# Optimization experiments

Hardware: AMD Instinct MI355X
Metric: run time of the kernel (lower is better)

## Reference

```python
import jax, jax.numpy as jnp
import numpy as np

ALPHA = jnp.full((8,), 0.25, dtype=jnp.float32)  # per-class focal alpha
GAMMA = 2.0
TEMP = 0.07
CIRC_TARGET = 1.0
CIRC_WEIGHT = 0.1
MIN_AGREE = 0.6
W_FOCAL, W_CONTRAST, W_CONSENSUS = 1.0, 0.5, 0.3


def setup_inputs() -> dict:
    key = jax.random.key(0)
    k1, k2, k3, k4, k5 = jax.random.split(key, 5)
    return {
        "logits": jax.random.normal(k1, (32, 8, 256, 256), dtype=jnp.float32),
        "target": jax.random.randint(k2, (32, 256, 256), 0, 8, dtype=jnp.int32),
        "features": jax.random.normal(k3, (1024, 512), dtype=jnp.float32),
        "masks": jax.random.uniform(k4, (32, 3, 256, 256), dtype=jnp.float32),
        "method_preds": jax.random.uniform(k5, (3, 32, 256, 256), dtype=jnp.float32),
    }


def focal_loss(logits, target):
    B, C, H, W = logits.shape
    x = logits.transpose(0, 2, 3, 1).reshape(-1, C)  # [BHW, C]
    t = target.reshape(-1)
    logp = jax.nn.log_softmax(x, axis=-1)
    ce = -jnp.take_along_axis(logp, t[:, None], axis=1)[:, 0]
    p = jnp.exp(-ce)
    focal_w = ALPHA[t] * (1.0 - p) ** GAMMA
    return jnp.mean(focal_w * ce)


def contrastive_loss(features):
    Bf = features.shape[0]
    f = features / jnp.linalg.norm(features, axis=1, keepdims=True)
    sim = (f @ f.T) / TEMP  # [Bf, Bf]
    # default labels = arange(Bf//2) tiled twice -> each sample has exactly one
    # positive: its paired view at index (i + Bf//2) % Bf
    pos_idx = (jnp.arange(Bf) + Bf // 2) % Bf
    pos = sim[jnp.arange(Bf), pos_idx]
    diag = jnp.eye(Bf, dtype=bool)
    # logits row i = {positive_i} U negatives_i = all j != i (single positive case)
    masked = jnp.where(diag, -1e30, sim)
    lse = jax.nn.logsumexp(masked, axis=1)
    return jnp.mean(lse - pos)  # CE with target = the (only) positive


def circularity_loss(masks):
    m = masks[:, 0]  # [B, H, W] core channel
    B = m.shape[0]
    area = jnp.sum(m, axis=(1, 2))
    ex = jnp.sum(jnp.abs(m[:, 1:, :] - m[:, :-1, :]), axis=(1, 2))
    ey = jnp.sum(jnp.abs(m[:, :, 1:] - m[:, :, :-1]), axis=(1, 2))
    per = ex + ey
    circ = 4.0 * np.pi * area / jnp.maximum(per, 1e-12) ** 2
    li = jnp.where((area > 0) & (per > 0), (circ - CIRC_TARGET) ** 2, 0.0)
    return CIRC_WEIGHT * jnp.sum(li) / B


def consensus_loss(method_preds):
    K = method_preds.shape[0]
    total, n = 0.0, 0
    for i in range(K):  # K=3 methods -> 3 pairs (fixed, small)
        for j in range(i + 1, K):
            pi, pj = method_preds[i], method_preds[j]
            inter = jnp.sum(pi * pj)
            union = jnp.sum(pi + pj - pi * pj)
            iou = inter / (union + 1e-6)
            total = total + jax.nn.relu(MIN_AGREE - iou)
            n += 1
    return total / n


def reference(logits, target, features, masks, method_preds):
    return (W_FOCAL * focal_loss(logits, target)
            + W_CONTRAST * contrastive_loss(features)
            + circularity_loss(masks)
            + W_CONSENSUS * consensus_loss(method_preds))
```

## Files before the change

kernel.cpp:

```cpp
#include <hip/hip_runtime.h>
#include <math.h>

#define WS_FOCALP 0
#define WS_CONSP  2048
#define WS_AREAP  14336
#define WS_EXP_   14848
#define WS_EYP_   15360
#define WS_POS    15872
#define WS_PART   16896
#define WS_HI_B   393216
#define WS_LO_B   1441792

typedef __attribute__((ext_vector_type(8))) short bf16x8;
typedef __attribute__((ext_vector_type(4))) float f32x4;

#define MFMA16(a, b, c) __builtin_amdgcn_mfma_f32_16x16x32_bf16((a), (b), (c), 0, 0, 0)

__device__ inline float wave_reduce(float v) {
#pragma unroll
  for (int m = 32; m >= 1; m >>= 1) v += __shfl_xor(v, m);
  return v;
}

__device__ inline unsigned short bf16_rne(float x) {
  union { float f; unsigned u; } v; v.f = x;
  unsigned r = v.u + 0x7FFF + ((v.u >> 16) & 1);
  return (unsigned short)(r >> 16);
}
__device__ inline float bf16_f(unsigned short h) {
  union { unsigned u; float f; } v; v.u = ((unsigned)h) << 16; return v.f;
}

__device__ inline float focal_px(float v0, float v1, float v2, float v3,
                                 float v4, float v5, float v6, float v7, int tt) {
  float mx = fmaxf(fmaxf(fmaxf(v0, v1), fmaxf(v2, v3)),
                   fmaxf(fmaxf(v4, v5), fmaxf(v6, v7)));
  float se = __expf(v0 - mx) + __expf(v1 - mx) + __expf(v2 - mx) + __expf(v3 - mx) +
             __expf(v4 - mx) + __expf(v5 - mx) + __expf(v6 - mx) + __expf(v7 - mx);
  float xt = v0;
  xt = (tt == 1) ? v1 : xt;
  xt = (tt == 2) ? v2 : xt;
  xt = (tt == 3) ? v3 : xt;
  xt = (tt == 4) ? v4 : xt;
  xt = (tt == 5) ? v5 : xt;
  xt = (tt == 6) ? v6 : xt;
  xt = (tt == 7) ? v7 : xt;
  float lp = (xt - mx) - __logf(se);
  float p = __expf(lp);
  float om = 1.0f - p;
  return 0.25f * om * om * (-lp);
}

__global__ __launch_bounds__(256) void mega_kernel(
    const float* __restrict__ logits, const int* __restrict__ target,
    const float* __restrict__ feat, const float* __restrict__ masks,
    const float* __restrict__ preds, float* __restrict__ ws) {
  __shared__ float red[32];
  const int bid = blockIdx.x;
  const int tid = threadIdx.x;
  const int lane = tid & 63;
  const int wid = tid >> 6;

  if (bid < 2048) {
    int t = bid * 256 + tid;
    int p4 = t * 4;
    int b = p4 >> 16;
    int hw = p4 & 65535;
    const float* lb = logits + (b << 19) + hw;
    float4 x0 = *(const float4*)(lb + (0 << 16));
    float4 x1 = *(const float4*)(lb + (1 << 16));
    float4 x2 = *(const float4*)(lb + (2 << 16));
    float4 x3 = *(const float4*)(lb + (3 << 16));
    float4 x4 = *(const float4*)(lb + (4 << 16));
    float4 x5 = *(const float4*)(lb + (5 << 16));
    float4 x6 = *(const float4*)(lb + (6 << 16));
    float4 x7 = *(const float4*)(lb + (7 << 16));
    int4 tg = *(const int4*)(target + p4);
    float acc = 0.0f;
    acc += focal_px(x0.x, x1.x, x2.x, x3.x, x4.x, x5.x, x6.x, x7.x, tg.x);
    acc += focal_px(x0.y, x1.y, x2.y, x3.y, x4.y, x5.y, x6.y, x7.y, tg.y);
    acc += focal_px(x0.z, x1.z, x2.z, x3.z, x4.z, x5.z, x6.z, x7.z, tg.z);
    acc += focal_px(x0.w, x1.w, x2.w, x3.w, x4.w, x5.w, x6.w, x7.w, tg.w);
    float v = wave_reduce(acc);
    if (lane == 0) red[wid] = v;
    __syncthreads();
    if (tid == 0) ws[WS_FOCALP + bid] = red[0] + red[1] + red[2] + red[3];

  } else if (bid < 2560) {
    int bi = bid - 2048;
    int img = bi >> 4;
    int part = bi & 15;
    const float* mS = masks + img * 3 * 65536;
    const float4* m4 = (const float4*)mS;
    float a = 0.0f, ex = 0.0f, ey = 0.0f;
#pragma unroll
    for (int i = 0; i < 4; i++) {
      int v = tid + 256 * i;
      int rl = v >> 6;
      int c4 = v & 63;
      int row = part * 16 + rl;
      float4 val = m4[row * 64 + c4];
      a += val.x + val.y + val.z + val.w;
      ey += fabsf(val.y - val.x) + fabsf(val.z - val.y) + fabsf(val.w - val.z);
      if (c4 > 0) ey += fabsf(val.x - mS[row * 256 + c4 * 4 - 1]);
      if (row > 0) {
        float4 u = m4[(row - 1) * 64 + c4];
        ex += fabsf(val.x - u.x) + fabsf(val.y - u.y) +
              fabsf(val.z - u.z) + fabsf(val.w - u.w);
      }
    }
    float ra = wave_reduce(a);
    float rx = wave_reduce(ex);
    float ry = wave_reduce(ey);
    if (lane == 0) {
      red[wid + 0] = ra; red[wid + 4] = rx; red[wid + 8] = ry;
    }
    __syncthreads();
    if (tid == 0) {
      ws[WS_AREAP + bi] = red[0] + red[1] + red[2] + red[3];
      ws[WS_EXP_ + bi] = red[4] + red[5] + red[6] + red[7];
      ws[WS_EYP_ + bi] = red[8] + red[9] + red[10] + red[11];
    }

  } else if (bid < 4608) {
    int b = bid - 2560;
    int t = b * 256 + tid;
    const float4* q = (const float4*)preds;
    float4 a0 = q[t];
    float4 a1 = q[t + 524288];
    float4 a2 = q[t + 1048576];
    float s0 = a0.x + a0.y + a0.z + a0.w;
    float s1 = a1.x + a1.y + a1.z + a1.w;
    float s2 = a2.x + a2.y + a2.z + a2.w;
    float p01 = a0.x * a1.x + a0.y * a1.y + a0.z * a1.z + a0.w * a1.w;
    float p02 = a0.x * a2.x + a0.y * a2.y + a0.z * a2.z + a0.w * a2.w;
    float p12 = a1.x * a2.x + a1.y * a2.y + a1.z * a2.z + a1.w * a2.w;
    float r0 = wave_reduce(s0);
    float r1 = wave_reduce(s1);
    float r2 = wave_reduce(s2);
    float r3 = wave_reduce(p01);
    float r4 = wave_reduce(p02);
    float r5 = wave_reduce(p12);
    if (lane == 0) {
      red[wid + 0] = r0; red[wid + 4] = r1; red[wid + 8] = r2;
      red[wid + 12] = r3; red[wid + 16] = r4; red[wid + 20] = r5;
    }
    __syncthreads();
    if (tid == 0) {
#pragma unroll
      for (int k = 0; k < 6; k++)
        ws[WS_CONSP + k * 2048 + b] =
            red[k * 4] + red[k * 4 + 1] + red[k * 4 + 2] + red[k * 4 + 3];
    }

  } else {
    int row = (bid - 4608) * 4 + wid;
    const float4* f4 = (const float4*)feat;
    float4 u = f4[row * 128 + lane];
    float4 w = f4[row * 128 + 64 + lane];
    float s = u.x * u.x + u.y * u.y + u.z * u.z + u.w * u.w +
              w.x * w.x + w.y * w.y + w.z * w.z + w.w * w.w;
    s = wave_reduce(s);
    float scale = 3.7796447300922719f / sqrtf(s);
    float g[8] = {u.x * scale, u.y * scale, u.z * scale, u.w * scale,
                  w.x * scale, w.y * scale, w.z * scale, w.w * scale};
    unsigned short h[8];
    unsigned short l[8];
#pragma unroll
    for (int i = 0; i < 8; i++) {
      h[i] = bf16_rne(g[i]);
      l[i] = bf16_rne(g[i] - bf16_f(h[i]));
    }
    const int rg = row >> 4, r15 = row & 15;
    int k0 = lane * 4;
    int k1 = 256 + lane * 4;
    int off0 = (rg * 16 + (k0 >> 5)) * 1024 + (((k0 >> 3) & 3) * 16 + r15) * 16 + (k0 & 7) * 2;
    int off1 = (rg * 16 + (k1 >> 5)) * 1024 + (((k1 >> 3) & 3) * 16 + r15) * 16 + (k1 & 7) * 2;
    char* hb = (char*)ws + WS_HI_B;
    char* lb = (char*)ws + WS_LO_B;
    *(ushort4*)(hb + off0) = make_ushort4(h[0], h[1], h[2], h[3]);
    *(ushort4*)(hb + off1) = make_ushort4(h[4], h[5], h[6], h[7]);
    *(ushort4*)(lb + off0) = make_ushort4(l[0], l[1], l[2], l[3]);
    *(ushort4*)(lb + off1) = make_ushort4(l[4], l[5], l[6], l[7]);
  }
}

__global__ __launch_bounds__(256) void sim_kernel(float* __restrict__ ws) {
  const int tid = threadIdx.x;
  const int lane = tid & 63;
  const int wid = tid >> 6;
  const int rt = blockIdx.x >> 4, ct = blockIdx.x & 15;
  const int wr = wid >> 1, wc = wid & 1;
  const int l15 = lane & 15;
  const int hi8 = lane >> 4;
  const char* HI = (const char*)ws + WS_HI_B;
  const char* LO = (const char*)ws + WS_LO_B;
  const int rga = rt * 2 + wr;
  const int rgb = ct * 4 + wc * 2;
  const int lb16 = lane * 16;
  const char* pAh = HI + rga * 16384 + lb16;
  const char* pAl = LO + rga * 16384 + lb16;
  const char* pB0h = HI + rgb * 16384 + lb16;
  const char* pB0l = LO + rgb * 16384 + lb16;
  const char* pB1h = HI + (rgb + 1) * 16384 + lb16;
  const char* pB1l = LO + (rgb + 1) * 16384 + lb16;

  f32x4 acc0 = {0.f, 0.f, 0.f, 0.f};
  f32x4 acc1 = {0.f, 0.f, 0.f, 0.f};

  bf16x8 Aah0, Aal0, Abh00, Abl00, Abh10, Abl10;
  bf16x8 Aah1, Aal1, Abh01, Abl01, Abh11, Abl11;
  bf16x8 Bah0, Bal0, Bbh00, Bbl00, Bbh10, Bbl10;
  bf16x8 Bah1, Bal1, Bbh01, Bbl01, Bbh11, Bbl11;

#define LOADP(P, K0)                                                     \
  do {                                                                   \
    int o0 = (K0) * 1024, o1 = (K0) * 1024 + 1024;                       \
    P##ah0 = *(const bf16x8*)(pAh + o0);                                 \
    P##ah1 = *(const bf16x8*)(pAh + o1);                                 \
    P##al0 = *(const bf16x8*)(pAl + o0);                                 \
    P##al1 = *(const bf16x8*)(pAl + o1);                                 \
    P##bh00 = *(const bf16x8*)(pB0h + o0);                               \
    P##bh01 = *(const bf16x8*)(pB0h + o1);                               \
    P##bl00 = *(const bf16x8*)(pB0l + o0);                               \
    P##bl01 = *(const bf16x8*)(pB0l + o1);                               \
    P##bh10 = *(const bf16x8*)(pB1h + o0);                               \
    P##bh11 = *(const bf16x8*)(pB1h + o1);                               \
    P##bl10 = *(const bf16x8*)(pB1l + o0);                               \
    P##bl11 = *(const bf16x8*)(pB1l + o1);                               \
  } while (0)

#define MFMAP(P)                                                         \
  do {                                                                   \
    acc0 = MFMA16(P##ah0, P##bh00, acc0);                                \
    acc1 = MFMA16(P##ah0, P##bh10, acc1);                                \
    acc0 = MFMA16(P##ah0, P##bl00, acc0);                                \
    acc1 = MFMA16(P##ah0, P##bl10, acc1);                                \
    acc0 = MFMA16(P##al0, P##bh00, acc0);                                \
    acc1 = MFMA16(P##al0, P##bh10, acc1);                                \
    acc0 = MFMA16(P##ah1, P##bh01, acc0);                                \
    acc1 = MFMA16(P##ah1, P##bh11, acc1);                                \
    acc0 = MFMA16(P##ah1, P##bl01, acc0);                                \
    acc1 = MFMA16(P##ah1, P##bl11, acc1);                                \
    acc0 = MFMA16(P##al1, P##bh01, acc0);                                \
    acc1 = MFMA16(P##al1, P##bh11, acc1);                                \
  } while (0)

  LOADP(A, 0);
#pragma unroll 1
  for (int kb = 0; kb < 12; kb += 4) {
    LOADP(B, kb + 2);
    __builtin_amdgcn_sched_barrier(0);
    MFMAP(A);
    LOADP(A, kb + 4);
    __builtin_amdgcn_sched_barrier(0);
    MFMAP(B);
  }
  LOADP(B, 14);
  __builtin_amdgcn_sched_barrier(0);
  MFMAP(A);
  MFMAP(B);

#undef LOADP
#undef MFMAP

  float2* part = (float2*)(ws + WS_PART);
  int c0 = ct * 64 + wc * 32 + l15;
  int c1 = c0 + 16;
#pragma unroll
  for (int q = 0; q < 4; q++) {
    int row = rt * 32 + wr * 16 + hi8 * 4 + q;
    int pc = (row + 512) & 1023;
    float v0 = acc0[q], v1 = acc1[q];
    if (c0 == pc) ws[WS_POS + row] = v0;
    if (c1 == pc) ws[WS_POS + row] = v1;
    if (c0 == row) v0 = -1e30f;
    if (c1 == row) v1 = -1e30f;
    float m = fmaxf(v0, v1);
    float s = __expf(v0 - m) + __expf(v1 - m);
#pragma unroll
    for (int d = 1; d < 16; d <<= 1) {
      float mo = __shfl_xor(m, d), so = __shfl_xor(s, d);
      float nm = fmaxf(m, mo);
      s = s * __expf(m - nm) + so * __expf(mo - nm);
      m = nm;
    }
    if (l15 == 0) part[row * 32 + ct * 2 + wc] = make_float2(m, s);
  }
}

__global__ __launch_bounds__(1024) void final_kernel(float* __restrict__ ws,
                                                     float* __restrict__ out) {
  __shared__ float red[16][8];
  __shared__ float li_s[32];
  int r = threadIdx.x;
  int lane = r & 63, wid = r >> 6;

  float v[8];
  const float2* part = (const float2*)(ws + WS_PART);
  float M = -1e30f, S = 0.0f;
#pragma unroll
  for (int ctl = 0; ctl < 32; ctl++) {
    float2 p = part[r * 32 + ctl];
    float nm = fmaxf(M, p.x);
    S = S * __expf(M - nm) + p.y * __expf(p.x - nm);
    M = nm;
  }
  v[0] = (M + __logf(S)) - ws[WS_POS + r];
  v[1] = ws[WS_FOCALP + r] + ws[WS_FOCALP + r + 1024];
#pragma unroll
  for (int k = 0; k < 6; k++) {
    const float* p = ws + WS_CONSP + k * 2048;
    v[2 + k] = p[r] + p[r + 1024];
  }
#pragma unroll
  for (int k = 0; k < 8; k++) {
    v[k] = wave_reduce(v[k]);
    if (lane == 0) red[wid][k] = v[k];
  }

  if (r < 512) {
    float a = ws[WS_AREAP + r];
    float ex = ws[WS_EXP_ + r];
    float ey = ws[WS_EYP_ + r];
#pragma unroll
    for (int d = 1; d < 16; d <<= 1) {
      a += __shfl_xor(a, d);
      ex += __shfl_xor(ex, d);
      ey += __shfl_xor(ey, d);
    }
    if ((r & 15) == 0) {
      float per = ex + ey;
      float dd = fmaxf(per, 1e-12f);
      float c = 12.566370614359172f * a / (dd * dd);
      li_s[r >> 4] = (a > 0.0f && per > 0.0f) ? (c - 1.0f) * (c - 1.0f) : 0.0f;
    }
  }
  __syncthreads();

  if (r == 0) {
    float tot[8];
#pragma unroll
    for (int k = 0; k < 8; k++) {
      float t = 0.0f;
#pragma unroll
      for (int i = 0; i < 16; i++) t += red[i][k];
      tot[k] = t;
    }
    float circ = 0.0f;
#pragma unroll
    for (int i = 0; i < 32; i++) circ += li_s[i];
    circ = 0.1f * circ / 32.0f;

    float contr = tot[0] / 1024.0f;
    float focal = tot[1] / 2097152.0f;

    float S0 = tot[2], S1 = tot[3], S2 = tot[4];
    float P01 = tot[5], P02 = tot[6], P12 = tot[7];
    float co = 0.0f;
    co += fmaxf(0.6f - P01 / (S0 + S1 - P01 + 1e-6f), 0.0f);
    co += fmaxf(0.6f - P02 / (S0 + S2 - P02 + 1e-6f), 0.0f);
    co += fmaxf(0.6f - P12 / (S1 + S2 - P12 + 1e-6f), 0.0f);
    co *= (1.0f / 3.0f);

    out[0] = focal + 0.5f * contr + circ + 0.3f * co;
  }
}

extern "C" void kernel_launch(void* const* d_in, const int* in_sizes, int n_in,
                              void* d_out, int out_size, void* d_ws, size_t ws_size,
                              hipStream_t stream) {
  const float* logits = (const float*)d_in[0];
  const int* target = (const int*)d_in[1];
  const float* feat = (const float*)d_in[2];
  const float* masks = (const float*)d_in[3];
  const float* preds = (const float*)d_in[4];
  float* ws = (float*)d_ws;
  float* out = (float*)d_out;

  mega_kernel<<<4864, 256, 0, stream>>>(logits, target, feat, masks, preds, ws);
  sim_kernel<<<512, 256, 0, stream>>>(ws);
  final_kernel<<<1, 1024, 0, stream>>>(ws, out);
}
```

Before: 47.53 us.

## Split feature prep into own kernel and fuse sim GEMM with streaming reductions

```diff
diff --git a/kernel.cpp b/kernel.cpp
--- a/kernel.cpp
+++ b/kernel.cpp
@@ -8,8 +8,8 @@
 #define WS_EYP_   15360
 #define WS_POS    15872
 #define WS_PART   16896
-#define WS_HI_B   393216
-#define WS_LO_B   1441792
+#define WS_HI_B   1048576
+#define WS_LO_B   2621440
 
 typedef __attribute__((ext_vector_type(8))) short bf16x8;
 typedef __attribute__((ext_vector_type(4))) float f32x4;
@@ -51,18 +51,157 @@
   return 0.25f * om * om * (-lp);
 }
 
-__global__ __launch_bounds__(256) void mega_kernel(
+__global__ __launch_bounds__(256) void prep_kernel(const float* __restrict__ feat,
+                                                   float* __restrict__ ws) {
+  const int tid = threadIdx.x;
+  const int lane = tid & 63;
+  const int wid = tid >> 6;
+  int row = blockIdx.x * 4 + wid;
+  const float4* f4 = (const float4*)feat;
+  float4 u = f4[row * 128 + lane];
+  float4 w = f4[row * 128 + 64 + lane];
+  float s = u.x * u.x + u.y * u.y + u.z * u.z + u.w * u.w +
+            w.x * w.x + w.y * w.y + w.z * w.z + w.w * w.w;
+  s = wave_reduce(s);
+  float scale = 3.7796447300922719f / sqrtf(s);
+  float g[8] = {u.x * scale, u.y * scale, u.z * scale, u.w * scale,
+                w.x * scale, w.y * scale, w.z * scale, w.w * scale};
+  unsigned short h[8];
+  unsigned short l[8];
+#pragma unroll
+  for (int i = 0; i < 8; i++) {
+    h[i] = bf16_rne(g[i]);
+    l[i] = bf16_rne(g[i] - bf16_f(h[i]));
+  }
+  const int rg = row >> 4, r15 = row & 15;
+  int k0 = lane * 4;
+  int k1 = 256 + lane * 4;
+  int off0 = (rg * 16 + (k0 >> 5)) * 1024 + (((k0 >> 3) & 3) * 16 + r15) * 16 + (k0 & 7) * 2;
+  int off1 = (rg * 16 + (k1 >> 5)) * 1024 + (((k1 >> 3) & 3) * 16 + r15) * 16 + (k1 & 7) * 2;
+  char* hb = (char*)ws + WS_HI_B;
+  char* lb = (char*)ws + WS_LO_B;
+  *(ushort4*)(hb + off0) = make_ushort4(h[0], h[1], h[2], h[3]);
+  *(ushort4*)(hb + off1) = make_ushort4(h[4], h[5], h[6], h[7]);
+  *(ushort4*)(lb + off0) = make_ushort4(l[0], l[1], l[2], l[3]);
+  *(ushort4*)(lb + off1) = make_ushort4(l[4], l[5], l[6], l[7]);
+}
+
+__global__ __launch_bounds__(256, 1) void fused_kernel(
     const float* __restrict__ logits, const int* __restrict__ target,
-    const float* __restrict__ feat, const float* __restrict__ masks,
-    const float* __restrict__ preds, float* __restrict__ ws) {
+    const float* __restrict__ masks, const float* __restrict__ preds,
+    float* __restrict__ ws) {
   __shared__ float red[32];
   const int bid = blockIdx.x;
   const int tid = threadIdx.x;
   const int lane = tid & 63;
   const int wid = tid >> 6;
 
-  if (bid < 2048) {
-    int t = bid * 256 + tid;
+  if (bid < 512) {
+    const int rt = bid >> 4, ct = bid & 15;
+    const int wr = wid >> 1, wc = wid & 1;
+    const int l15 = lane & 15;
+    const int hi8 = lane >> 4;
+    const char* HI = (const char*)ws + WS_HI_B;
+    const char* LO = (const char*)ws + WS_LO_B;
+    const int rga = rt * 2 + wr;
+    const int rgb = ct * 4 + wc * 2;
+    const int lb16 = lane * 16;
+    const char* pAh = HI + rga * 16384 + lb16;
+    const char* pAl = LO + rga * 16384 + lb16;
+    const char* pB0h = HI + rgb * 16384 + lb16;
+    const char* pB0l = LO + rgb * 16384 + lb16;
+    const char* pB1h = HI + (rgb + 1) * 16384 + lb16;
+    const char* pB1l = LO + (rgb + 1) * 16384 + lb16;
+
+    f32x4 acc0 = {0.f, 0.f, 0.f, 0.f};
+    f32x4 acc1 = {0.f, 0.f, 0.f, 0.f};
+
+    bf16x8 Aah0, Aal0, Abh00, Abl00, Abh10, Abl10;
+    bf16x8 Aah1, Aal1, Abh01, Abl01, Abh11, Abl11;
+    bf16x8 Bah0, Bal0, Bbh00, Bbl00, Bbh10, Bbl10;
+    bf16x8 Bah1, Bal1, Bbh01, Bbl01, Bbh11, Bbl11;
+
+#define LOADP(P, K0)                                                     \
+  do {                                                                   \
+    int o0 = (K0) * 1024, o1 = (K0) * 1024 + 1024;                       \
+    P##ah0 = *(const bf16x8*)(pAh + o0);                                 \
+    P##ah1 = *(const bf16x8*)(pAh + o1);                                 \
+    P##al0 = *(const bf16x8*)(pAl + o0);                                 \
+    P##al1 = *(const bf16x8*)(pAl + o1);                                 \
+    P##bh00 = *(const bf16x8*)(pB0h + o0);                               \
+    P##bh01 = *(const bf16x8*)(pB0h + o1);                               \
+    P##bl00 = *(const bf16x8*)(pB0l + o0);                               \
+    P##bl01 = *(const bf16x8*)(pB0l + o1);                               \
+    P##bh10 = *(const bf16x8*)(pB1h + o0);                               \
+    P##bh11 = *(const bf16x8*)(pB1h + o1);                               \
+    P##bl10 = *(const bf16x8*)(pB1l + o0);                               \
+    P##bl11 = *(const bf16x8*)(pB1l + o1);                               \
+  } while (0)
+
+#define MFMAP(P)                                                         \
+  do {                                                                   \
+    acc0 = MFMA16(P##ah0, P##bh00, acc0);                                \
+    acc1 = MFMA16(P##ah0, P##bh10, acc1);                                \
+    acc0 = MFMA16(P##ah0, P##bl00, acc0);                                \
+    acc1 = MFMA16(P##ah0, P##bl10, acc1);                                \
+    acc0 = MFMA16(P##al0, P##bh00, acc0);                                \
+    acc1 = MFMA16(P##al0, P##bh10, acc1);                                \
+    acc0 = MFMA16(P##ah1, P##bh01, acc0);                                \
+    acc1 = MFMA16(P##ah1, P##bh11, acc1);                                \
+    acc0 = MFMA16(P##ah1, P##bl01, acc0);                                \
+    acc1 = MFMA16(P##ah1, P##bl11, acc1);                                \
+    acc0 = MFMA16(P##al1, P##bh01, acc0);                                \
+    acc1 = MFMA16(P##al1, P##bh11, acc1);                                \
+  } while (0)
+
+    LOADP(A, 0);
+#pragma unroll 1
+    for (int kb = 0; kb < 12; kb += 4) {
+      LOADP(B, kb + 2);
+      __builtin_amdgcn_sched_barrier(0);
+      MFMAP(A);
+      LOADP(A, kb + 4);
+      __builtin_amdgcn_sched_barrier(0);
+      MFMAP(B);
+    }
+    LOADP(B, 14);
+    __builtin_amdgcn_sched_barrier(0);
+    MFMAP(A);
+    MFMAP(B);
+
+#undef LOADP
+#undef MFMAP
+
+    float2* part = (float2*)(ws + WS_PART);
+    int c0 = ct * 64 + wc * 32 + l15;
+    int c1 = c0 + 16;
+#pragma unroll
+    for (int q = 0; q < 4; q++) {
+      int row = rt * 32 + wr * 16 + hi8 * 4 + q;
+      int pc = (row + 512) & 1023;
+      float v0 = acc0[q], v1 = acc1[q];
+      if (c0 == pc) ws[WS_POS + row] = v0;
+      if (c1 == pc) ws[WS_POS + row] = v1;
+      if (c0 == row) v0 = -1e30f;
+      if (c1 == row) v1 = -1e30f;
+      float m = fmaxf(v0, v1);
+      float s = __expf(v0 - m) + __expf(v1 - m);
+#pragma unroll
+      for (int d = 1; d < 16; d <<= 1) {
+        float mo = __shfl_xor(m, d), so = __shfl_xor(s, d);
+        float nm = fmaxf(m, mo);
+        s = s * __expf(m - nm) + so * __expf(mo - nm);
+        m = nm;
+      }
+      if (l15 == 0) part[row * 32 + ct * 2 + wc] = make_float2(m, s);
+    }
+    return;
+  }
+
+  const int bid2 = bid - 512;
+
+  if (bid2 < 2048) {
+    int t = bid2 * 256 + tid;
     int p4 = t * 4;
     int b = p4 >> 16;
     int hw = p4 & 65535;
@@ -84,10 +223,10 @@
     float v = wave_reduce(acc);
     if (lane == 0) red[wid] = v;
     __syncthreads();
-    if (tid == 0) ws[WS_FOCALP + bid] = red[0] + red[1] + red[2] + red[3];
-
-  } else if (bid < 2560) {
-    int bi = bid - 2048;
+    if (tid == 0) ws[WS_FOCALP + bid2] = red[0] + red[1] + red[2] + red[3];
+
+  } else if (bid2 < 2560) {
+    int bi = bid2 - 2048;
     int img = bi >> 4;
     int part = bi & 15;
     const float* mS = masks + img * 3 * 65536;
@@ -122,8 +261,8 @@
       ws[WS_EYP_ + bi] = red[8] + red[9] + red[10] + red[11];
     }
 
-  } else if (bid < 4608) {
-    int b = bid - 2560;
+  } else {
+    int b = bid2 - 2560;
     int t = b * 256 + tid;
     const float4* q = (const float4*)preds;
     float4 a0 = q[t];
@@ -152,140 +291,6 @@
         ws[WS_CONSP + k * 2048 + b] =
             red[k * 4] + red[k * 4 + 1] + red[k * 4 + 2] + red[k * 4 + 3];
     }
-
-  } else {
-    int row = (bid - 4608) * 4 + wid;
-    const float4* f4 = (const float4*)feat;
-    float4 u = f4[row * 128 + lane];
-    float4 w = f4[row * 128 + 64 + lane];
-    float s = u.x * u.x + u.y * u.y + u.z * u.z + u.w * u.w +
-              w.x * w.x + w.y * w.y + w.z * w.z + w.w * w.w;
-    s = wave_reduce(s);
-    float scale = 3.7796447300922719f / sqrtf(s);
-    float g[8] = {u.x * scale, u.y * scale, u.z * scale, u.w * scale,
-                  w.x * scale, w.y * scale, w.z * scale, w.w * scale};
-    unsigned short h[8];
-    unsigned short l[8];
-#pragma unroll
-    for (int i = 0; i < 8; i++) {
-      h[i] = bf16_rne(g[i]);
-      l[i] = bf16_rne(g[i] - bf16_f(h[i]));
-    }
-    const int rg = row >> 4, r15 = row & 15;
-    int k0 = lane * 4;
-    int k1 = 256 + lane * 4;
-    int off0 = (rg * 16 + (k0 >> 5)) * 1024 + (((k0 >> 3) & 3) * 16 + r15) * 16 + (k0 & 7) * 2;
-    int off1 = (rg * 16 + (k1 >> 5)) * 1024 + (((k1 >> 3) & 3) * 16 + r15) * 16 + (k1 & 7) * 2;
-    char* hb = (char*)ws + WS_HI_B;
-    char* lb = (char*)ws + WS_LO_B;
-    *(ushort4*)(hb + off0) = make_ushort4(h[0], h[1], h[2], h[3]);
-    *(ushort4*)(hb + off1) = make_ushort4(h[4], h[5], h[6], h[7]);
-    *(ushort4*)(lb + off0) = make_ushort4(l[0], l[1], l[2], l[3]);
-    *(ushort4*)(lb + off1) = make_ushort4(l[4], l[5], l[6], l[7]);
-  }
-}
-
-__global__ __launch_bounds__(256) void sim_kernel(float* __restrict__ ws) {
-  const int tid = threadIdx.x;
-  const int lane = tid & 63;
-  const int wid = tid >> 6;
-  const int rt = blockIdx.x >> 4, ct = blockIdx.x & 15;
-  const int wr = wid >> 1, wc = wid & 1;
-  const int l15 = lane & 15;
-  const int hi8 = lane >> 4;
-  const char* HI = (const char*)ws + WS_HI_B;
-  const char* LO = (const char*)ws + WS_LO_B;
-  const int rga = rt * 2 + wr;
-  const int rgb = ct * 4 + wc * 2;
-  const int lb16 = lane * 16;
-  const char* pAh = HI + rga * 16384 + lb16;
-  const char* pAl = LO + rga * 16384 + lb16;
-  const char* pB0h = HI + rgb * 16384 + lb16;
-  const char* pB0l = LO + rgb * 16384 + lb16;
-  const char* pB1h = HI + (rgb + 1) * 16384 + lb16;
-  const char* pB1l = LO + (rgb + 1) * 16384 + lb16;
-
-  f32x4 acc0 = {0.f, 0.f, 0.f, 0.f};
-  f32x4 acc1 = {0.f, 0.f, 0.f, 0.f};
-
-  bf16x8 Aah0, Aal0, Abh00, Abl00, Abh10, Abl10;
-  bf16x8 Aah1, Aal1, Abh01, Abl01, Abh11, Abl11;
-  bf16x8 Bah0, Bal0, Bbh00, Bbl00, Bbh10, Bbl10;
-  bf16x8 Bah1, Bal1, Bbh01, Bbl01, Bbh11, Bbl11;
-
-#define LOADP(P, K0)                                                     \
-  do {                                                                   \
-    int o0 = (K0) * 1024, o1 = (K0) * 1024 + 1024;                       \
-    P##ah0 = *(const bf16x8*)(pAh + o0);                                 \
-    P##ah1 = *(const bf16x8*)(pAh + o1);                                 \
-    P##al0 = *(const bf16x8*)(pAl + o0);                                 \
-    P##al1 = *(const bf16x8*)(pAl + o1);                                 \
-    P##bh00 = *(const bf16x8*)(pB0h + o0);                               \
-    P##bh01 = *(const bf16x8*)(pB0h + o1);                               \
-    P##bl00 = *(const bf16x8*)(pB0l + o0);                               \
-    P##bl01 = *(const bf16x8*)(pB0l + o1);                               \
-    P##bh10 = *(const bf16x8*)(pB1h + o0);                               \
-    P##bh11 = *(const bf16x8*)(pB1h + o1);                               \
-    P##bl10 = *(const bf16x8*)(pB1l + o0);                               \
-    P##bl11 = *(const bf16x8*)(pB1l + o1);                               \
-  } while (0)
-
-#define MFMAP(P)                                                         \
-  do {                                                                   \
-    acc0 = MFMA16(P##ah0, P##bh00, acc0);                                \
-    acc1 = MFMA16(P##ah0, P##bh10, acc1);                                \
-    acc0 = MFMA16(P##ah0, P##bl00, acc0);                                \
-    acc1 = MFMA16(P##ah0, P##bl10, acc1);                                \
-    acc0 = MFMA16(P##al0, P##bh00, acc0);                                \
-    acc1 = MFMA16(P##al0, P##bh10, acc1);                                \
-    acc0 = MFMA16(P##ah1, P##bh01, acc0);                                \
-    acc1 = MFMA16(P##ah1, P##bh11, acc1);                                \
-    acc0 = MFMA16(P##ah1, P##bl01, acc0);                                \
-    acc1 = MFMA16(P##ah1, P##bl11, acc1);                                \
-    acc0 = MFMA16(P##al1, P##bh01, acc0);                                \
-    acc1 = MFMA16(P##al1, P##bh11, acc1);                                \
-  } while (0)
-
-  LOADP(A, 0);
-#pragma unroll 1
-  for (int kb = 0; kb < 12; kb += 4) {
-    LOADP(B, kb + 2);
-    __builtin_amdgcn_sched_barrier(0);
-    MFMAP(A);
-    LOADP(A, kb + 4);
-    __builtin_amdgcn_sched_barrier(0);
-    MFMAP(B);
-  }
-  LOADP(B, 14);
-  __builtin_amdgcn_sched_barrier(0);
-  MFMAP(A);
-  MFMAP(B);
-
-#undef LOADP
-#undef MFMAP
-
-  float2* part = (float2*)(ws + WS_PART);
-  int c0 = ct * 64 + wc * 32 + l15;
-  int c1 = c0 + 16;
-#pragma unroll
-  for (int q = 0; q < 4; q++) {
-    int row = rt * 32 + wr * 16 + hi8 * 4 + q;
-    int pc = (row + 512) & 1023;
-    float v0 = acc0[q], v1 = acc1[q];
-    if (c0 == pc) ws[WS_POS + row] = v0;
-    if (c1 == pc) ws[WS_POS + row] = v1;
-    if (c0 == row) v0 = -1e30f;
-    if (c1 == row) v1 = -1e30f;
-    float m = fmaxf(v0, v1);
-    float s = __expf(v0 - m) + __expf(v1 - m);
-#pragma unroll
-    for (int d = 1; d < 16; d <<= 1) {
-      float mo = __shfl_xor(m, d), so = __shfl_xor(s, d);
-      float nm = fmaxf(m, mo);
-      s = s * __expf(m - nm) + so * __expf(mo - nm);
-      m = nm;
-    }
-    if (l15 == 0) part[row * 32 + ct * 2 + wc] = make_float2(m, s);
   }
 }
 
@@ -378,7 +383,7 @@
   float* ws = (float*)d_ws;
   float* out = (float*)d_out;
 
-  mega_kernel<<<4864, 256, 0, stream>>>(logits, target, feat, masks, preds, ws);
-  sim_kernel<<<512, 256, 0, stream>>>(ws);
+  prep_kernel<<<256, 256, 0, stream>>>(feat, ws);
+  fused_kernel<<<5120, 256, 0, stream>>>(logits, target, masks, preds, ws);
   final_kernel<<<1, 1024, 0, stream>>>(ws, out);
 }
```

Result: no change. 47.98 us (+0.9%).
